# Performance work log

Measured on AMD Instinct MI355X. Metric: run time of the kernel, lower is better.

Reference implementation:

```python
import jax, jax.numpy as jnp
import numpy as np

K, T, CIN = 30000, 35, 7
EPS = 1e-5  # torch BatchNorm default


def _bn(x, gamma, beta):
    # x: [1, K, T, C]; per-channel batch-stat normalization over (0,1,2)
    mean = jnp.mean(x, axis=(0, 1, 2))
    var = jnp.var(x, axis=(0, 1, 2))
    return (x - mean) * jax.lax.rsqrt(var + EPS) * gamma + beta


def _vfe(x, mask, W, b, gamma, beta):
    # x: [1, K, T, Cin] -> [1, K, T, 2*units]
    pw = jnp.einsum('bkti,iu->bktu', x, W) + b
    pw = jax.nn.relu(_bn(pw, gamma, beta))
    agg = jnp.max(pw, axis=2, keepdims=True)            # [1, K, 1, units]
    out = jnp.concatenate([pw, jnp.broadcast_to(agg, pw.shape)], axis=-1)
    return out * mask


def setup_inputs() -> dict:
    key = jax.random.key(0)
    ks = jax.random.split(key, 8)
    inp = {}
    inp['x'] = jax.random.normal(ks[0], (K, T, CIN), jnp.float32)
    inp['coordinate'] = jax.random.randint(ks[1], (K, 4), 0, 1, dtype=jnp.int32)
    inp['batch_size'] = 1
    inp['W1'] = jax.random.normal(ks[2], (7, 16), jnp.float32) * 0.3
    inp['b1'] = jnp.zeros((16,), jnp.float32)
    inp['g1'] = jnp.ones((16,), jnp.float32)
    inp['be1'] = jnp.zeros((16,), jnp.float32)
    inp['W2'] = jax.random.normal(ks[3], (32, 64), jnp.float32) * 0.15
    inp['b2'] = jnp.zeros((64,), jnp.float32)
    inp['g2'] = jnp.ones((64,), jnp.float32)
    inp['be2'] = jnp.zeros((64,), jnp.float32)
    inp['Wd'] = jax.random.normal(ks[4], (128, 128), jnp.float32) * 0.1
    inp['bd'] = jnp.zeros((128,), jnp.float32)
    inp['gd'] = jnp.ones((128,), jnp.float32)
    inp['bed'] = jnp.zeros((128,), jnp.float32)
    return inp


def reference(x, coordinate, batch_size, W1, b1, g1, be1, W2, b2, g2, be2, Wd, bd, gd, bed):
    xb = x[None]                                   # [1, K, T, 7]
    # mask: 1 where the point's feature sum is nonzero
    mask = (jnp.sum(xb, axis=-1) != 0.0).astype(jnp.float32)[..., None]  # [1,K,T,1]
    h = _vfe(xb, mask, W1, b1, g1, be1)            # [1, K, T, 32]
    h = _vfe(h, mask, W2, b2, g2, be2)             # [1, K, T, 128]
    h = jnp.einsum('bktc,cd->bktd', h, Wd) + bd    # [1, K, T, 128]
    h = _bn(h, gd, bed)                            # BatchNorm2d after permute(0,3,1,2)
    h = jnp.where(h >= 0, h, 0.1 * h)              # leaky_relu(0.1)
    h = jnp.max(h, axis=2)                         # max over points -> [1, K, 128]
    out = jnp.transpose(h, (0, 2, 1))              # [1, 128, K] to match NCHW layout
    return (out, coordinate)
```

## Files before the change

kernel.cpp:

```cpp
#include <hip/hip_runtime.h>

#define KVOX 30000
#define TP 35
#define NPTS (KVOX * TP)
#define EPS_BN 1e-5f

typedef __attribute__((ext_vector_type(8))) short short8_t;
typedef __attribute__((ext_vector_type(4))) float f32x4;

#define MFMA_BF16 __builtin_amdgcn_mfma_f32_16x16x32_bf16

#define SLOTG_OFF 0
#define SLOT2_OFF 2560
#define SLOT3_OFF 10752
#define PAR_A1 27136
#define PAR_C1 27152
#define PAR_A2 27168
#define PAR_C2 27232
#define PAR_A3 27296
#define PAR_C3 27424
#define STATS_FLOATS 27136
#define W2T_OFF 27552
#define WDT_OFF 28576
#define M3_OFF 36768
#define SMALL_FLOATS (36768 + KVOX * 64)
#define H1G_OFF SMALL_FLOATS
#define REC_DW 1224
#define FULL_FLOATS (H1G_OFF + (KVOX / 4) * REC_DW)

__device__ __forceinline__ ushort f2bf(float f) {
    uint r;
    asm("v_cvt_pk_bf16_f32 %0, %1, %2" : "=v"(r) : "v"(f), "v"(f));
    return (ushort)r;
}
__device__ __forceinline__ uint f2bf2(float lo, float hi) {
    uint r;
    asm("v_cvt_pk_bf16_f32 %0, %1, %2" : "=v"(r) : "v"(lo), "v"(hi));
    return r;
}
__device__ __forceinline__ float bf2f(ushort h) {
    union { uint u; float f; } v; v.u = ((uint)h) << 16; return v.f;
}

__global__ __launch_bounds__(256) void k_prep_stats1(
    const float* __restrict__ x,
    const float* __restrict__ W2, const float* __restrict__ Wd,
    const float* __restrict__ gd,
    ushort* __restrict__ w2t, ushort* __restrict__ wdt,
    float* __restrict__ slotG) {
    if (blockIdx.x < 64) {
        int t = blockIdx.x * 256 + threadIdx.x;
        if (t < 2048) {
            int u = t >> 5, k = t & 31;
            w2t[t] = f2bf(W2[k * 64 + u]);
        }
        int u = t >> 7, k = t & 127;
        float sg = (gd[u] < 0.f) ? -1.f : 1.f;
        wdt[t] = f2bf(Wd[k * 128 + u] * sg);
        return;
    }
    int bid = blockIdx.x - 64;
    int tid = threadIdx.x;
    int gid = bid * 256 + tid;
    float sx[7], G[28];
#pragma unroll
    for (int c = 0; c < 7; ++c) sx[c] = 0.f;
#pragma unroll
    for (int i = 0; i < 28; ++i) G[i] = 0.f;
    for (size_t p4 = (size_t)gid * 4; p4 < NPTS; p4 += (size_t)65536 * 4) {
        const f32x4* xp = (const f32x4*)(x + p4 * 7);
        f32x4 q[7];
#pragma unroll
        for (int c = 0; c < 7; ++c) q[c] = xp[c];
#pragma unroll
        for (int j = 0; j < 4; ++j) {
            float xv[7];
#pragma unroll
            for (int c = 0; c < 7; ++c) {
                int idx = j * 7 + c;
                xv[c] = q[idx >> 2][idx & 3];
                sx[c] += xv[c];
            }
            int idx = 0;
#pragma unroll
            for (int i = 0; i < 7; ++i)
#pragma unroll
                for (int jj = i; jj < 7; ++jj) { G[idx] = fmaf(xv[i], xv[jj], G[idx]); ++idx; }
        }
    }
    int lane = tid & 63;
    int wv = tid >> 6;
    int slot = (bid * 4 + wv) & 63;
#pragma unroll
    for (int k = 0; k < 35; ++k) {
        float v = (k < 28) ? G[k] : sx[k - 28];
#pragma unroll
        for (int m = 32; m > 0; m >>= 1) v += __shfl_xor(v, m, 64);
        if (lane == 0) atomicAdd(&slotG[slot * 40 + k], v);
    }
}

__global__ void k_affine1g(const float* __restrict__ slotG,
                           const float* __restrict__ W1, const float* __restrict__ b1,
                           const float* __restrict__ g1, const float* __restrict__ be1,
                           float* __restrict__ pa, float* __restrict__ pc, float invN) {
    __shared__ float red[35];
    int t = threadIdx.x;
    if (t < 35) {
        float s = 0.f;
#pragma unroll
        for (int sl = 0; sl < 64; ++sl) s += slotG[sl * 40 + t];
        red[t] = s;
    }
    __syncthreads();
    if (t < 16) {
        float wv[7];
#pragma unroll
        for (int c = 0; c < 7; ++c) wv[c] = W1[c * 16 + t];
        float b = b1[t];
        float sw = 0.f;
#pragma unroll
        for (int c = 0; c < 7; ++c) sw = fmaf(red[28 + c], wv[c], sw);
        float gq = 0.f;
        int idx = 0;
#pragma unroll
        for (int i = 0; i < 7; ++i)
#pragma unroll
            for (int j = i; j < 7; ++j) {
                float coef = wv[i] * wv[j];
                if (i != j) coef *= 2.f;
                gq = fmaf(coef, red[idx], gq);
                ++idx;
            }
        float mr = sw * invN;
        float mean = mr + b;
        float ex2 = gq * invN + 2.f * b * mr + b * b;
        float var = ex2 - mean * mean;
        float av = g1[t] * rsqrtf(var + EPS_BN);
        pa[t] = av;
        pc[t] = be1[t] - mean * av;
    }
}

__global__ void k_affine_b(const float* __restrict__ slots,
                           const float* __restrict__ g,
                           const float* __restrict__ be,
                           const float* __restrict__ bias,
                           float* __restrict__ pa, float* __restrict__ pc,
                           int C, float invN) {
    int u = threadIdx.x;
    if (u >= C) return;
    float s = 0.f, q = 0.f;
    for (int sl = 0; sl < 64; ++sl) {
        s += slots[sl * 2 * C + u];
        q += slots[sl * 2 * C + C + u];
    }
    float b = bias[u];
    float mr = s * invN;
    float mean = mr + b;
    float ex2 = q * invN + 2.f * b * mr + b * b;
    float var = ex2 - mean * mean;
    float av = g[u] * rsqrtf(var + EPS_BN);
    pa[u] = av;
    pc[u] = be[u] - mean * av;
}

__global__ void k_affine_b3(const float* __restrict__ slots,
                            const float* __restrict__ g,
                            const float* __restrict__ be,
                            const float* __restrict__ bias,
                            float* __restrict__ pa, float* __restrict__ pc,
                            int C, float invN) {
    int u = threadIdx.x;
    if (u >= C) return;
    float s = 0.f, q = 0.f;
    for (int sl = 0; sl < 64; ++sl) {
        s += slots[sl * 2 * C + u];
        q += slots[sl * 2 * C + C + u];
    }
    float sg = (g[u] < 0.f) ? -1.f : 1.f;
    s *= sg;
    float b = bias[u];
    float mr = s * invN;
    float mean = mr + b;
    float ex2 = q * invN + 2.f * b * mr + b * b;
    float var = ex2 - mean * mean;
    float av = g[u] * rsqrtf(var + EPS_BN);
    pa[u] = av;
    pc[u] = be[u] - mean * av;
}

__device__ __forceinline__ void phaseA4(
    int k0, int tid,
    const float* __restrict__ x,
    const float* __restrict__ W1, const float* __restrict__ b1,
    const float* __restrict__ a1, const float* __restrict__ c1,
    ushort* __restrict__ h1, float* __restrict__ lmask,
    float* __restrict__ aggp , ushort* __restrict__ agg1bf ) {
    int u = tid & 15;
    int g = tid >> 4;
    int v = g & 3;
    int th = g >> 2;
    float pmax = 0.f;
    if (th < 7) {
        float b1u = b1[u];
        float a1u = a1[u], c1u = c1[u];
        float w1c[7];
#pragma unroll
        for (int c = 0; c < 7; ++c) w1c[c] = W1[c * 16 + u];
#pragma unroll
        for (int i = 0; i < 5; ++i) {
            int t = th * 5 + i;
            const float* xp = x + ((size_t)(k0 + v) * TP + t) * 7;
            float xv[7];
            float sum7 = 0.f;
#pragma unroll
            for (int c = 0; c < 7; ++c) { xv[c] = xp[c]; sum7 += xv[c]; }
            float mkv = (sum7 != 0.f) ? 1.f : 0.f;
            int row = 4 * t + v;
            if (u == 0) lmask[row] = mkv;
            float val = b1u;
#pragma unroll
            for (int c = 0; c < 7; ++c) val = fmaf(xv[c], w1c[c], val);
            val = fmaxf(fmaf(a1u, val, c1u), 0.f);
            pmax = fmaxf(pmax, val);
            h1[row * 24 + u] = f2bf(val * mkv);
        }
    } else {
        int row = 140 + v;
        h1[row * 24 + u] = 0;
        if (u == 0) lmask[row] = 0.f;
    }
    int w = tid >> 6;
    int lane = tid & 63;
    if (w < 7) aggp[w * 64 + lane] = pmax;
    __syncthreads();
    if (tid < 64) {
        float m = aggp[tid];
#pragma unroll
        for (int ww = 1; ww < 7; ++ww) m = fmaxf(m, aggp[ww * 64 + tid]);
        agg1bf[tid] = f2bf(m);
    }
    __syncthreads();
}

template <bool DUMP>
__global__ __launch_bounds__(512, 8) void k_stats2(
    const float* __restrict__ x,
    const float* __restrict__ W1, const float* __restrict__ b1,
    const ushort* __restrict__ w2t,
    const float* __restrict__ ws,
    float* __restrict__ slot2, uint* __restrict__ recs) {
    __shared__ __align__(16) ushort h1[144 * 24];
    __shared__ float lmask[144];
    __shared__ float aggp[7 * 64];
    __shared__ __align__(16) ushort agg1bf[64];
    __shared__ __align__(16) uint zeros16[4];
    int tid = threadIdx.x;
    int k0 = blockIdx.x * 4;
    if (tid < 4) zeros16[tid] = 0;
    phaseA4(k0, tid, x, W1, b1, ws + PAR_A1, ws + PAR_C1, h1, lmask, aggp, agg1bf);
    if (DUMP) {
        uint* rec = recs + (size_t)blockIdx.x * REC_DW;
        const uint* h1dw = (const uint*)h1;
        for (int i = tid; i < 1120; i += 512) rec[i] = h1dw[(i >> 3) * 12 + (i & 7)];
        if (tid < 32) rec[1120 + tid] = ((const uint*)agg1bf)[tid];
        if (tid < 70) rec[1152 + tid] = f2bf2(lmask[2 * tid], lmask[2 * tid + 1]);
    }
    int w = tid >> 6, lane = tid & 63, lq = lane >> 4, lr = lane & 15;
    int mh = w >> 2, uq = w & 3;
    int u = uq * 16 + lr;
    short8_t bB = *(const short8_t*)(w2t + u * 32 + (lq & 1) * 8);
    short8_t bP = *(const short8_t*)(w2t + u * 32 + 16 + (lq & 1) * 8);
    const ushort* pap = (lq < 2) ? (agg1bf + (lr & 3) * 16 + (lq & 1) * 8) : (const ushort*)zeros16;
    short8_t pAf = *(const short8_t*)pap;
    f32x4 aP = {0.f, 0.f, 0.f, 0.f};
    aP = MFMA_BF16(pAf, bP, aP, 0, 0, 0);
    f32x4 p1;
    p1[0] = __shfl(aP[0], lr, 64); p1[1] = __shfl(aP[1], lr, 64);
    p1[2] = __shfl(aP[2], lr, 64); p1[3] = __shfl(aP[3], lr, 64);
    f32x4 s1p = {0.f, 0.f, 0.f, 0.f}, s2p = {0.f, 0.f, 0.f, 0.f};
    int mt0 = mh ? 5 : 0, mt1 = mh ? 9 : 5;
    for (int mt = mt0; mt < mt1; ++mt) {
        const ushort* ha = (lq < 2) ? (h1 + (mt * 16 + lr) * 24 + (lq & 1) * 8) : (const ushort*)zeros16;
        short8_t af = *(const short8_t*)ha;
        f32x4 acc = {0.f, 0.f, 0.f, 0.f};
        acc = MFMA_BF16(af, bB, acc, 0, 0, 0);
        f32x4 mk = *(const f32x4*)(lmask + mt * 16 + lq * 4);
        f32x4 am = (acc + p1) * mk;
        s1p += am;
        s2p += am * am;
    }
    float s1 = s1p[0] + s1p[1] + s1p[2] + s1p[3];
    float s2 = s2p[0] + s2p[1] + s2p[2] + s2p[3];
    s1 += __shfl_xor(s1, 16, 64); s1 += __shfl_xor(s1, 32, 64);
    s2 += __shfl_xor(s2, 16, 64); s2 += __shfl_xor(s2, 32, 64);
    if (lq == 0) {
        int slot = blockIdx.x & 63;
        atomicAdd(&slot2[slot * 128 + u], s1);
        atomicAdd(&slot2[slot * 128 + 64 + u], s2);
    }
}

__global__ __launch_bounds__(512, 8) void k_stage3_reuse(
    const uint* __restrict__ recs,
    const float* __restrict__ b2,
    const ushort* __restrict__ w2t, const ushort* __restrict__ wdt,
    const float* __restrict__ bd, const float* __restrict__ gd,
    const float* __restrict__ ws,
    float* __restrict__ slot3, ushort* __restrict__ m3) {
    __shared__ __align__(16) ushort h1[144 * 24];
    __shared__ __align__(16) ushort h2[144 * 72];
    __shared__ float lmask[144];
    __shared__ __align__(16) uint aggfU[4 * 68];
    __shared__ __align__(16) ushort agg1bf[64];
    __shared__ __align__(16) uint zeros16[4];
    int tid = threadIdx.x;
    int k0 = blockIdx.x * 4;
    int w = tid >> 6, lane = tid & 63, lq = lane >> 4, lr = lane & 15;

    {
        const uint* rec = recs + (size_t)blockIdx.x * REC_DW;
        uint* h1dw = (uint*)h1;
        {
            int i = tid;              h1dw[(i >> 3) * 12 + (i & 7)] = rec[i];
            i = tid + 512;            h1dw[(i >> 3) * 12 + (i & 7)] = rec[i];
            i = tid + 1024; if (i < 1120) h1dw[(i >> 3) * 12 + (i & 7)] = rec[i];
        }
        if (tid < 48) h1dw[140 * 12 + tid] = 0u;
        if (tid < 32) ((uint*)agg1bf)[tid] = rec[1120 + tid];
        if (tid < 72) {
            if (tid < 70) {
                uint mw = rec[1152 + tid];
                lmask[2 * tid] = bf2f((ushort)(mw & 0xffffu));
                lmask[2 * tid + 1] = bf2f((ushort)(mw >> 16));
            } else {
                int j = 140 + (tid - 70) * 2;
                lmask[j] = 0.f; lmask[j + 1] = 0.f;
            }
        }
        if (tid < 272) aggfU[tid] = 0u;
        if (tid < 4) zeros16[tid] = 0u;
    }
    __syncthreads();

    {
        int mh = w >> 2, uq = w & 3;
        int u = uq * 16 + lr;
        short8_t bB = *(const short8_t*)(w2t + u * 32 + (lq & 1) * 8);
        short8_t bP = *(const short8_t*)(w2t + u * 32 + 16 + (lq & 1) * 8);
        const ushort* pap = (lq < 2) ? (agg1bf + (lr & 3) * 16 + (lq & 1) * 8) : (const ushort*)zeros16;
        short8_t pAf = *(const short8_t*)pap;
        f32x4 aP = {0.f, 0.f, 0.f, 0.f};
        aP = MFMA_BF16(pAf, bP, aP, 0, 0, 0);
        f32x4 p1;
        p1[0] = __shfl(aP[0], lr, 64); p1[1] = __shfl(aP[1], lr, 64);
        p1[2] = __shfl(aP[2], lr, 64); p1[3] = __shfl(aP[3], lr, 64);
        float a2u = ws[PAR_A2 + u];
        float c2u = fmaf(a2u, b2[u], ws[PAR_C2 + u]);
        f32x4 av = {0.f, 0.f, 0.f, 0.f};
        int mt0 = mh ? 5 : 0, mt1 = mh ? 9 : 5;
        for (int mt = mt0; mt < mt1; ++mt) {
            const ushort* ha = (lq < 2) ? (h1 + (mt * 16 + lr) * 24 + (lq & 1) * 8) : (const ushort*)zeros16;
            short8_t af = *(const short8_t*)ha;
            f32x4 acc = {0.f, 0.f, 0.f, 0.f};
            acc = MFMA_BF16(af, bB, acc, 0, 0, 0);
            f32x4 mk = *(const f32x4*)(lmask + mt * 16 + lq * 4);
            int m0 = mt * 16 + lq * 4;
            f32x4 vals;
#pragma unroll
            for (int r = 0; r < 4; ++r) {
                float am = (acc[r] + p1[r]) * mk[r];
                float val = fmaxf(fmaf(a2u, am, c2u), 0.f);
                h2[(m0 + r) * 72 + u] = f2bf(val);
                vals[r] = val;
            }
            if (!(mt == 8 && lq == 3)) {
#pragma unroll
                for (int r = 0; r < 4; ++r) av[r] = fmaxf(av[r], vals[r]);
            }
        }
#pragma unroll
        for (int r = 0; r < 4; ++r) {
            av[r] = fmaxf(av[r], __shfl_xor(av[r], 16, 64));
            av[r] = fmaxf(av[r], __shfl_xor(av[r], 32, 64));
        }
        if (lq == 0) {
#pragma unroll
            for (int r = 0; r < 4; ++r)
                atomicMax(&aggfU[r * 68 + u], __float_as_uint(av[r]));
        }
    }
    __syncthreads();

    {
        int u = w * 16 + lr;
        short8_t bM0 = *(const short8_t*)(wdt + u * 128 + lq * 8);
        short8_t bM1 = *(const short8_t*)(wdt + u * 128 + 32 + lq * 8);
        short8_t bP0 = *(const short8_t*)(wdt + u * 128 + 64 + lq * 8);
        short8_t bP1 = *(const short8_t*)(wdt + u * 128 + 96 + lq * 8);
        const float* aggf = (const float*)aggfU;
        f32x4 q0 = *(const f32x4*)(aggf + (lr & 3) * 68 + lq * 8);
        f32x4 q1 = *(const f32x4*)(aggf + (lr & 3) * 68 + lq * 8 + 4);
        f32x4 q2 = *(const f32x4*)(aggf + (lr & 3) * 68 + 32 + lq * 8);
        f32x4 q3 = *(const f32x4*)(aggf + (lr & 3) * 68 + 32 + lq * 8 + 4);
        union { uint uu[4]; short8_t s8; } pc0, pc1;
        pc0.uu[0] = f2bf2(q0[0], q0[1]); pc0.uu[1] = f2bf2(q0[2], q0[3]);
        pc0.uu[2] = f2bf2(q1[0], q1[1]); pc0.uu[3] = f2bf2(q1[2], q1[3]);
        pc1.uu[0] = f2bf2(q2[0], q2[1]); pc1.uu[1] = f2bf2(q2[2], q2[3]);
        pc1.uu[2] = f2bf2(q3[0], q3[1]); pc1.uu[3] = f2bf2(q3[2], q3[3]);
        f32x4 aP = {0.f, 0.f, 0.f, 0.f};
        aP = MFMA_BF16(pc0.s8, bP0, aP, 0, 0, 0);
        aP = MFMA_BF16(pc1.s8, bP1, aP, 0, 0, 0);
        f32x4 p2;
        p2[0] = __shfl(aP[0], lr, 64); p2[1] = __shfl(aP[1], lr, 64);
        p2[2] = __shfl(aP[2], lr, 64); p2[3] = __shfl(aP[3], lr, 64);
        f32x4 s1p = {0.f, 0.f, 0.f, 0.f}, s2p = {0.f, 0.f, 0.f, 0.f};
        f32x4 mx = {-1e30f, -1e30f, -1e30f, -1e30f};
#pragma unroll
        for (int mt = 0; mt < 9; ++mt) {
            const ushort* hrow = h2 + (mt * 16 + lr) * 72;
            short8_t a0 = *(const short8_t*)(hrow + lq * 8);
            short8_t a1 = *(const short8_t*)(hrow + 32 + lq * 8);
            f32x4 acc = {0.f, 0.f, 0.f, 0.f};
            acc = MFMA_BF16(a0, bM0, acc, 0, 0, 0);
            acc = MFMA_BF16(a1, bM1, acc, 0, 0, 0);
            f32x4 mk = *(const f32x4*)(lmask + mt * 16 + lq * 4);
            f32x4 am = (acc + p2) * mk;
            s1p += am;
            s2p += am * am;
            if (mt < 8) {
#pragma unroll
                for (int r = 0; r < 4; ++r) mx[r] = fmaxf(mx[r], am[r]);
            } else if (lq < 3) {
#pragma unroll
                for (int r = 0; r < 4; ++r) mx[r] = fmaxf(mx[r], am[r]);
            }
        }
#pragma unroll
        for (int r = 0; r < 4; ++r) {
            mx[r] = fmaxf(mx[r], __shfl_xor(mx[r], 16, 64));
            mx[r] = fmaxf(mx[r], __shfl_xor(mx[r], 32, 64));
        }
        float s1 = s1p[0] + s1p[1] + s1p[2] + s1p[3];
        float s2 = s2p[0] + s2p[1] + s2p[2] + s2p[3];
        s1 += __shfl_xor(s1, 16, 64); s1 += __shfl_xor(s1, 32, 64);
        s2 += __shfl_xor(s2, 16, 64); s2 += __shfl_xor(s2, 32, 64);
        if (lq == 0) {
            float sg = (gd[u] < 0.f) ? -1.f : 1.f;
            float bdu = bd[u];
#pragma unroll
            for (int r = 0; r < 4; ++r)
                m3[(size_t)(k0 + r) * 128 + u] = f2bf(fmaf(sg, mx[r], bdu));
            int slot = blockIdx.x & 63;
            atomicAdd(&slot3[slot * 256 + u], s1);
            atomicAdd(&slot3[slot * 256 + 128 + u], s2);
        }
    }
}

__device__ __forceinline__ void phaseA_leg(
    int k0, int tid,
    const float* __restrict__ x,
    const float* __restrict__ W1, const float* __restrict__ b1,
    const float* __restrict__ a1, const float* __restrict__ c1,
    ushort* __restrict__ h1, float* __restrict__ lmask, float* __restrict__ aggp) {
    int u = tid & 15;
    int g = tid >> 4;
    int v = g & 1;
    int th = g >> 1;
    float pmax = 0.f;
    if (th < 7) {
        float b1u = b1[u];
        float a1u = a1[u], c1u = c1[u];
        float w1c[7];
#pragma unroll
        for (int c = 0; c < 7; ++c) w1c[c] = W1[c * 16 + u];
#pragma unroll
        for (int i = 0; i < 5; ++i) {
            int t = th * 5 + i;
            const float* xp = x + ((size_t)(k0 + v) * TP + t) * 7;
            float xv[7];
            float sum7 = 0.f;
#pragma unroll
            for (int c = 0; c < 7; ++c) { xv[c] = xp[c]; sum7 += xv[c]; }
            float mkv = (sum7 != 0.f) ? 1.f : 0.f;
            if (u == 0) lmask[v * TP + t] = mkv;
            float val = b1u;
#pragma unroll
            for (int c = 0; c < 7; ++c) val = fmaf(xv[c], w1c[c], val);
            val = fmaxf(fmaf(a1u, val, c1u), 0.f);
            pmax = fmaxf(pmax, val);
            h1[(v * TP + t) * 40 + u] = f2bf(val * mkv);
        }
    } else {
#pragma unroll
        for (int i = 0; i < 5; ++i) {
            int row = 70 + (g & 1) * 5 + i;
            h1[row * 40 + u] = 0;
            if (u == 0) lmask[row] = 0.f;
        }
    }
    pmax = fmaxf(pmax, __shfl_xor(pmax, 32, 64));
    int w = tid >> 6;
    int lane = tid & 63;
    if (lane < 32) aggp[w * 32 + lane] = pmax;
    __syncthreads();
    {
        int uu = tid & 15;
        int r0 = tid >> 4;
        float g0 = fmaxf(fmaxf(aggp[uu], aggp[32 + uu]),
                         fmaxf(aggp[64 + uu], aggp[96 + uu]));
        float g1 = fmaxf(fmaxf(aggp[16 + uu], aggp[48 + uu]),
                         fmaxf(aggp[80 + uu], aggp[112 + uu]));
        ushort a0 = f2bf(g0), a1b = f2bf(g1);
#pragma unroll
        for (int j = 0; j < 5; ++j) {
            int row = r0 + j * 16;
            float mkv = lmask[row];
            h1[row * 40 + 16 + uu] = (mkv != 0.f) ? ((row < TP) ? a0 : a1b) : (ushort)0;
        }
    }
    __syncthreads();
}

template <bool WSPATH>
__global__ __launch_bounds__(256) void k_stage3_full(
    const float* __restrict__ x,
    const float* __restrict__ W1, const float* __restrict__ b1,
    const float* __restrict__ b2,
    const ushort* __restrict__ w2t, const ushort* __restrict__ wdt,
    const float* __restrict__ bd, const float* __restrict__ gd,
    const float* __restrict__ ws,
    float* __restrict__ slot3,
    ushort* __restrict__ m3, float* __restrict__ outbuf) {
    __shared__ __align__(16) ushort h1[80 * 40];
    __shared__ __align__(16) ushort h2[80 * 136];
    __shared__ float lmask[80];
    __shared__ float aggp[128];
    __shared__ ushort agg2bf[128];
    int tid = threadIdx.x;
    int k0 = blockIdx.x * 2;
    int w = tid >> 6, lane = tid & 63, lq = lane >> 4, lr = lane & 15;
    phaseA_leg(k0, tid, x, W1, b1, ws + PAR_A1, ws + PAR_C1, h1, lmask, aggp);

    int u0 = w * 32;
    short8_t bfr[2][4];
#pragma unroll
    for (int s = 0; s < 2; ++s)
#pragma unroll
        for (int kk = 0; kk < 4; ++kk)
            bfr[s][kk] = *(const short8_t*)(wdt + ((u0 + s * 16 + lr) * 128 + kk * 32 + lq * 8));

    {
        int u = w * 16 + lr;
        short8_t bfrag = *(const short8_t*)(w2t + u * 32 + lq * 8);
        float a2u = ws[PAR_A2 + u];
        float c2p = fmaf(a2u, b2[u], ws[PAR_C2 + u]);
        float aggv0 = 0.f, aggv1 = 0.f;
#pragma unroll
        for (int mt = 0; mt < 5; ++mt) {
            short8_t afrag = *(const short8_t*)(h1 + (mt * 16 + lr) * 40 + lq * 8);
            f32x4 acc = {0.f, 0.f, 0.f, 0.f};
            acc = MFMA_BF16(afrag, bfrag, acc, 0, 0, 0);
#pragma unroll
            for (int r = 0; r < 4; ++r) {
                int m = mt * 16 + lq * 4 + r;
                float val = fmaxf(fmaf(a2u, acc[r], c2p), 0.f);
                float vm = (m < 70) ? val : 0.f;
                if (m < TP) aggv0 = fmaxf(aggv0, vm); else aggv1 = fmaxf(aggv1, vm);
                h2[m * 136 + u] = f2bf(val * lmask[m]);
            }
        }
        aggv0 = fmaxf(aggv0, __shfl_xor(aggv0, 16, 64));
        aggv0 = fmaxf(aggv0, __shfl_xor(aggv0, 32, 64));
        aggv1 = fmaxf(aggv1, __shfl_xor(aggv1, 16, 64));
        aggv1 = fmaxf(aggv1, __shfl_xor(aggv1, 32, 64));
        if (lq == 0) {
            agg2bf[u] = f2bf(aggv0);
            agg2bf[64 + u] = f2bf(aggv1);
        }
    }
    __syncthreads();
    {
        int c = tid & 63;
        int r0 = tid >> 6;
        ushort a0 = agg2bf[c], a1v = agg2bf[64 + c];
#pragma unroll
        for (int j = 0; j < 20; ++j) {
            int row = r0 + j * 4;
            float mkv = lmask[row];
            h2[row * 136 + 64 + c] = (mkv != 0.f) ? ((row < TP) ? a0 : a1v) : (ushort)0;
        }
    }
    __syncthreads();
    {
        float mxa[2][2], s1a[2], s2a[2];
#pragma unroll
        for (int s = 0; s < 2; ++s) {
            s1a[s] = 0.f; s2a[s] = 0.f;
            mxa[s][0] = -1e30f; mxa[s][1] = -1e30f;
        }
#pragma unroll
        for (int mt = 0; mt < 5; ++mt) {
            short8_t af[4];
#pragma unroll
            for (int kk = 0; kk < 4; ++kk)
                af[kk] = *(const short8_t*)(h2 + (mt * 16 + lr) * 136 + kk * 32 + lq * 8);
#pragma unroll
            for (int s = 0; s < 2; ++s) {
                f32x4 acc = {0.f, 0.f, 0.f, 0.f};
#pragma unroll
                for (int kk = 0; kk < 4; ++kk)
                    acc = MFMA_BF16(af[kk], bfr[s][kk], acc, 0, 0, 0);
#pragma unroll
                for (int r = 0; r < 4; ++r) {
                    float a = acc[r];
                    s1a[s] += a;
                    s2a[s] = fmaf(a, a, s2a[s]);
                    int m = mt * 16 + lq * 4 + r;
                    if (mt <= 1) mxa[s][0] = fmaxf(mxa[s][0], a);
                    else if (mt == 3) mxa[s][1] = fmaxf(mxa[s][1], a);
                    else if (mt == 2) { if (m < TP) mxa[s][0] = fmaxf(mxa[s][0], a); else mxa[s][1] = fmaxf(mxa[s][1], a); }
                    else { if (m < 70) mxa[s][1] = fmaxf(mxa[s][1], a); }
                }
            }
        }
#pragma unroll
        for (int s = 0; s < 2; ++s) {
#pragma unroll
            for (int v = 0; v < 2; ++v) {
                mxa[s][v] = fmaxf(mxa[s][v], __shfl_xor(mxa[s][v], 16, 64));
                mxa[s][v] = fmaxf(mxa[s][v], __shfl_xor(mxa[s][v], 32, 64));
            }
            s1a[s] += __shfl_xor(s1a[s], 16, 64); s1a[s] += __shfl_xor(s1a[s], 32, 64);
            s2a[s] += __shfl_xor(s2a[s], 16, 64); s2a[s] += __shfl_xor(s2a[s], 32, 64);
        }
        if (lq == 0) {
            int slot = blockIdx.x & 63;
#pragma unroll
            for (int s = 0; s < 2; ++s) {
                int u = u0 + s * 16 + lr;
                float bdu = bd[u];
                float sg = (gd[u] < 0.f) ? -1.f : 1.f;
#pragma unroll
                for (int v = 0; v < 2; ++v) {
                    float res = fmaf(sg, mxa[s][v], bdu);
                    if (WSPATH) m3[(size_t)(k0 + v) * 128 + u] = f2bf(res);
                    else        outbuf[(size_t)u * KVOX + (k0 + v)] = res;
                }
                atomicAdd(&slot3[slot * 256 + u], s1a[s]);
                atomicAdd(&slot3[slot * 256 + 128 + u], s2a[s]);
            }
        }
    }
}

__global__ __launch_bounds__(256) void k_final_ws(const ushort* __restrict__ m3,
                                                  const float* __restrict__ ws,
                                                  float* __restrict__ out) {
    __shared__ float tile[32][33];
    int tx = threadIdx.x & 31;
    int ty = threadIdx.x >> 5;
    int v0 = blockIdx.x * 32;
    int u0 = blockIdx.y * 32;
    const float* a3 = ws + PAR_A3;
    const float* c3 = ws + PAR_C3;
#pragma unroll
    for (int r = ty; r < 32; r += 8) {
        int v = v0 + r, u = u0 + tx;
        float y = 0.f;
        if (v < KVOX) {
            float a = a3[u], c = c3[u];
            float val = bf2f(m3[(size_t)v * 128 + u]);
            y = a * val + c;
            y = (y >= 0.f) ? y : 0.1f * y;
        }
        tile[r][tx] = y;
    }
    __syncthreads();
#pragma unroll
    for (int r = ty; r < 32; r += 8) {
        int u = u0 + r, v = v0 + tx;
        if (v < KVOX) out[(size_t)u * KVOX + v] = tile[tx][r];
    }
}

__global__ __launch_bounds__(256) void k_final_inplace(const float* __restrict__ ws,
                                                       float* __restrict__ out) {
    int v = blockIdx.x * 256 + threadIdx.x;
    int u = blockIdx.y;
    if (v >= KVOX) return;
    float a = ws[PAR_A3 + u], c = ws[PAR_C3 + u];
    size_t idx = (size_t)u * KVOX + v;
    float y = a * out[idx] + c;
    out[idx] = (y >= 0.f) ? y : 0.1f * y;
}

extern "C" void kernel_launch(void* const* d_in, const int* in_sizes, int n_in,
                              void* d_out, int out_size, void* d_ws, size_t ws_size,
                              hipStream_t stream) {
    const float* x   = (const float*)d_in[0];
    const void*  coord = d_in[1];
    const float* W1  = (const float*)d_in[3];
    const float* b1  = (const float*)d_in[4];
    const float* g1  = (const float*)d_in[5];
    const float* be1 = (const float*)d_in[6];
    const float* W2  = (const float*)d_in[7];
    const float* b2  = (const float*)d_in[8];
    const float* g2  = (const float*)d_in[9];
    const float* be2 = (const float*)d_in[10];
    const float* Wd  = (const float*)d_in[11];
    const float* bd  = (const float*)d_in[12];
    const float* gd  = (const float*)d_in[13];
    const float* bed = (const float*)d_in[14];
    float* ws = (float*)d_ws;
    float* out = (float*)d_out;
    ushort* w2t = (ushort*)(ws + W2T_OFF);
    ushort* wdt = (ushort*)(ws + WDT_OFF);
    ushort* m3  = (ushort*)(ws + M3_OFF);
    uint* recs  = (uint*)(ws + H1G_OFF);

    size_t wsf = ws_size / 4;
    bool full = wsf >= (size_t)FULL_FLOATS;
    bool small = wsf >= (size_t)SMALL_FLOATS;
    const float invN = 1.f / (float)NPTS;

    hipMemsetAsync(d_ws, 0, (size_t)STATS_FLOATS * 4, stream);

    k_prep_stats1<<<64 + 256, 256, 0, stream>>>(x, W2, Wd, gd, w2t, wdt, ws + SLOTG_OFF);
    k_affine1g<<<1, 64, 0, stream>>>(ws + SLOTG_OFF, W1, b1, g1, be1, ws + PAR_A1, ws + PAR_C1, invN);
    if (full)
        k_stats2<true><<<KVOX / 4, 512, 0, stream>>>(x, W1, b1, w2t, ws, ws + SLOT2_OFF, recs);
    else
        k_stats2<false><<<KVOX / 4, 512, 0, stream>>>(x, W1, b1, w2t, ws, ws + SLOT2_OFF, recs);
    k_affine_b<<<1, 64, 0, stream>>>(ws + SLOT2_OFF, g2, be2, b2, ws + PAR_A2, ws + PAR_C2, 64, invN);

    if (full) {
        k_stage3_reuse<<<KVOX / 4, 512, 0, stream>>>(recs, b2, w2t, wdt, bd, gd, ws,
                                                     ws + SLOT3_OFF, m3);
        k_affine_b3<<<1, 128, 0, stream>>>(ws + SLOT3_OFF, gd, bed, bd, ws + PAR_A3, ws + PAR_C3, 128, invN);
        k_final_ws<<<dim3((KVOX + 31) / 32, 4), 256, 0, stream>>>(m3, ws, out);
    } else if (small) {
        k_stage3_full<true><<<KVOX / 2, 256, 0, stream>>>(x, W1, b1, b2, w2t, wdt, bd, gd, ws,
                                                          ws + SLOT3_OFF, m3, out);
        k_affine_b3<<<1, 128, 0, stream>>>(ws + SLOT3_OFF, gd, bed, bd, ws + PAR_A3, ws + PAR_C3, 128, invN);
        k_final_ws<<<dim3((KVOX + 31) / 32, 4), 256, 0, stream>>>(m3, ws, out);
    } else {
        k_stage3_full<false><<<KVOX / 2, 256, 0, stream>>>(x, W1, b1, b2, w2t, wdt, bd, gd, ws,
                                                           ws + SLOT3_OFF, m3, out);
        k_affine_b3<<<1, 128, 0, stream>>>(ws + SLOT3_OFF, gd, bed, bd, ws + PAR_A3, ws + PAR_C3, 128, invN);
        k_final_inplace<<<dim3((KVOX + 255) / 256, 128), 256, 0, stream>>>(ws, out);
    }
    hipMemcpyAsync((char*)d_out + (size_t)128 * KVOX * 4, coord,
                   (size_t)KVOX * 4 * sizeof(int), hipMemcpyDeviceToDevice, stream);
}
```

Before: 154.0 us.

## Fuse stats and stage kernels into one persistent kernel with grid barriers

```diff
diff --git a/kernel.cpp b/kernel.cpp
--- a/kernel.cpp
+++ b/kernel.cpp
@@ -4,6 +4,9 @@
 #define TP 35
 #define NPTS (KVOX * TP)
 #define EPS_BN 1e-5f
+#define NBLK 768
+#define GRP 10
+#define TOTG 7500
 
 typedef __attribute__((ext_vector_type(8))) short short8_t;
 typedef __attribute__((ext_vector_type(4))) float f32x4;
@@ -13,20 +16,20 @@
 #define SLOTG_OFF 0
 #define SLOT2_OFF 2560
 #define SLOT3_OFF 10752
-#define PAR_A1 27136
-#define PAR_C1 27152
-#define PAR_A2 27168
-#define PAR_C2 27232
-#define PAR_A3 27296
-#define PAR_C3 27424
-#define STATS_FLOATS 27136
-#define W2T_OFF 27552
-#define WDT_OFF 28576
-#define M3_OFF 36768
-#define SMALL_FLOATS (36768 + KVOX * 64)
-#define H1G_OFF SMALL_FLOATS
-#define REC_DW 1224
-#define FULL_FLOATS (H1G_OFF + (KVOX / 4) * REC_DW)
+#define BAR_OFF   27136
+#define PAR_A1 27152
+#define PAR_C1 27168
+#define PAR_A2 27184
+#define PAR_C2 27248
+#define PAR_A3 27312
+#define PAR_C3 27440
+#define STATS_FLOATS 27568
+#define W2T_OFF 27568
+#define WDT_OFF 28592
+#define M3_OFF 36784
+#define SMALL_FLOATS (36784 + KVOX * 64)
+#define RECS_OFF SMALL_FLOATS
+#define FULL_FLOATS (RECS_OFF + TOTG * 1120)
 
 __device__ __forceinline__ ushort f2bf(float f) {
     uint r;
@@ -41,25 +44,434 @@
 __device__ __forceinline__ float bf2f(ushort h) {
     union { uint u; float f; } v; v.u = ((uint)h) << 16; return v.f;
 }
-
-__global__ __launch_bounds__(256) void k_prep_stats1(
+__device__ __forceinline__ float aload(const float* p) {
+    return __hip_atomic_load(p, __ATOMIC_RELAXED, __HIP_MEMORY_SCOPE_AGENT);
+}
+__device__ __forceinline__ void gbar(uint* c, uint nblk) {
+    __syncthreads();
+    if (threadIdx.x == 0) {
+        __threadfence();
+        __hip_atomic_fetch_add(c, 1u, __ATOMIC_RELEASE, __HIP_MEMORY_SCOPE_AGENT);
+        while (__hip_atomic_load(c, __ATOMIC_ACQUIRE, __HIP_MEMORY_SCOPE_AGENT) < nblk)
+            __builtin_amdgcn_s_sleep(1);
+        __threadfence();
+    }
+    __syncthreads();
+}
+
+__global__ __launch_bounds__(256) void k_prep(const float* __restrict__ W2,
+                                              const float* __restrict__ Wd,
+                                              const float* __restrict__ gd,
+                                              ushort* __restrict__ w2t,
+                                              ushort* __restrict__ wdt) {
+    int t = blockIdx.x * 256 + threadIdx.x;
+    if (t < 2048) {
+        int u = t >> 5, k = t & 31;
+        w2t[t] = f2bf(W2[k * 64 + u]);
+    }
+    int u = t >> 7, k = t & 127;
+    float sg = (gd[u] < 0.f) ? -1.f : 1.f;
+    wdt[t] = f2bf(Wd[k * 128 + u] * sg);
+}
+
+__global__ __launch_bounds__(512, 8) void k_fused(
     const float* __restrict__ x,
-    const float* __restrict__ W2, const float* __restrict__ Wd,
-    const float* __restrict__ gd,
-    ushort* __restrict__ w2t, ushort* __restrict__ wdt,
-    float* __restrict__ slotG) {
-    if (blockIdx.x < 64) {
-        int t = blockIdx.x * 256 + threadIdx.x;
-        if (t < 2048) {
-            int u = t >> 5, k = t & 31;
-            w2t[t] = f2bf(W2[k * 64 + u]);
-        }
-        int u = t >> 7, k = t & 127;
-        float sg = (gd[u] < 0.f) ? -1.f : 1.f;
-        wdt[t] = f2bf(Wd[k * 128 + u] * sg);
-        return;
-    }
-    int bid = blockIdx.x - 64;
+    const float* __restrict__ W1, const float* __restrict__ b1,
+    const float* __restrict__ g1, const float* __restrict__ be1,
+    const float* __restrict__ b2, const float* __restrict__ g2,
+    const float* __restrict__ be2,
+    const ushort* __restrict__ w2t, const ushort* __restrict__ wdt,
+    const float* __restrict__ bd, const float* __restrict__ gd,
+    float* __restrict__ slotG, float* __restrict__ slot2,
+    float* __restrict__ slot3,
+    uint* __restrict__ bar, uint* __restrict__ recs,
+    ushort* __restrict__ m3) {
+    __shared__ __align__(16) ushort h1[144 * 24];
+    __shared__ __align__(16) ushort h2[144 * 72];
+    __shared__ __align__(16) float lmask[GRP][144];
+    __shared__ __align__(16) ushort agg1[GRP][64];
+    __shared__ __align__(16) uint aggfU[2][272];
+    __shared__ float parA1[16], parC1[16], parA2[64], parC2[64];
+    __shared__ __align__(16) uint zeros16[4];
+    float* aggp = (float*)h2;
+
+    const float invN = 1.f / (float)NPTS;
+    int tid = threadIdx.x;
+    int b = blockIdx.x;
+    int w = tid >> 6, lane = tid & 63, lq = lane >> 4, lr = lane & 15;
+
+    if (tid < 4) zeros16[tid] = 0u;
+    for (int j = tid; j < GRP * 144; j += 512) ((float*)lmask)[j] = 0.f;
+    if (tid < 64) h1[(140 + (tid >> 4)) * 24 + (tid & 15)] = 0;
+
+    {
+        float sx[7], G[28];
+#pragma unroll
+        for (int c = 0; c < 7; ++c) sx[c] = 0.f;
+#pragma unroll
+        for (int i = 0; i < 28; ++i) G[i] = 0.f;
+        int gid = b * 512 + tid;
+        if (gid < NPTS / 4) {
+            const float* xp = x + (size_t)gid * 28;
+#pragma unroll
+            for (int j = 0; j < 4; ++j) {
+                float xv[7];
+#pragma unroll
+                for (int c = 0; c < 7; ++c) { xv[c] = xp[j * 7 + c]; sx[c] += xv[c]; }
+                int idx = 0;
+#pragma unroll
+                for (int ii = 0; ii < 7; ++ii)
+#pragma unroll
+                    for (int jj = ii; jj < 7; ++jj) {
+                        G[idx] = fmaf(xv[ii], xv[jj], G[idx]); ++idx;
+                    }
+            }
+        }
+        int slot = (b * 8 + w) & 63;
+#pragma unroll
+        for (int k = 0; k < 35; ++k) {
+            float v = (k < 28) ? G[k] : sx[k - 28];
+#pragma unroll
+            for (int m = 32; m > 0; m >>= 1) v += __shfl_xor(v, m, 64);
+            if (lane == 0) atomicAdd(&slotG[slot * 40 + k], v);
+        }
+    }
+    gbar(&bar[0], NBLK);
+
+    if (tid < 35) {
+        float s = 0.f;
+#pragma unroll
+        for (int sl = 0; sl < 64; ++sl) s += aload(&slotG[sl * 40 + tid]);
+        aggp[tid] = s;
+    }
+    __syncthreads();
+    if (tid < 16) {
+        float wv[7];
+#pragma unroll
+        for (int c = 0; c < 7; ++c) wv[c] = W1[c * 16 + tid];
+        float bq = b1[tid];
+        float sw = 0.f;
+#pragma unroll
+        for (int c = 0; c < 7; ++c) sw = fmaf(aggp[28 + c], wv[c], sw);
+        float gq = 0.f;
+        int idx = 0;
+#pragma unroll
+        for (int ii = 0; ii < 7; ++ii)
+#pragma unroll
+            for (int jj = ii; jj < 7; ++jj) {
+                float coef = wv[ii] * wv[jj];
+                if (ii != jj) coef *= 2.f;
+                gq = fmaf(coef, aggp[idx], gq);
+                ++idx;
+            }
+        float mr = sw * invN;
+        float mean = mr + bq;
+        float ex2 = gq * invN + 2.f * bq * mr + bq * bq;
+        float var = ex2 - mean * mean;
+        float av = g1[tid] * rsqrtf(var + EPS_BN);
+        parA1[tid] = av;
+        parC1[tid] = be1[tid] - mean * av;
+    }
+    __syncthreads();
+
+    for (int i = 0; i < GRP; ++i) {
+        int g = b * GRP + i;
+        bool act = g < TOTG;
+        int k0 = g * 4;
+        if (act) {
+            int u = tid & 15, gg = tid >> 4, v = gg & 3, th = gg >> 2;
+            float pmax = 0.f;
+            if (th < 7) {
+                float b1u = b1[u];
+                float a1u = parA1[u], c1u = parC1[u];
+                float w1c[7];
+#pragma unroll
+                for (int c = 0; c < 7; ++c) w1c[c] = W1[c * 16 + u];
+#pragma unroll
+                for (int ii = 0; ii < 5; ++ii) {
+                    int t = th * 5 + ii;
+                    const float* xp = x + ((size_t)(k0 + v) * TP + t) * 7;
+                    float xv[7];
+                    float sum7 = 0.f;
+#pragma unroll
+                    for (int c = 0; c < 7; ++c) { xv[c] = xp[c]; sum7 += xv[c]; }
+                    float mkv = (sum7 != 0.f) ? 1.f : 0.f;
+                    int row = 4 * t + v;
+                    if (u == 0) lmask[i][row] = mkv;
+                    float val = b1u;
+#pragma unroll
+                    for (int c = 0; c < 7; ++c) val = fmaf(xv[c], w1c[c], val);
+                    val = fmaxf(fmaf(a1u, val, c1u), 0.f);
+                    pmax = fmaxf(pmax, val);
+                    h1[row * 24 + u] = f2bf(val * mkv);
+                }
+            }
+            if (w < 7) aggp[w * 64 + lane] = pmax;
+        }
+        __syncthreads();
+        if (act && tid < 64) {
+            float m = aggp[tid];
+#pragma unroll
+            for (int ww = 1; ww < 7; ++ww) m = fmaxf(m, aggp[ww * 64 + tid]);
+            agg1[i][tid] = f2bf(m);
+        }
+        __syncthreads();
+        if (act) {
+            const uint* h1dw = (const uint*)h1;
+            uint* rec = recs + (size_t)g * 1120;
+            {
+                int j = tid;            rec[j] = h1dw[(j >> 3) * 12 + (j & 7)];
+                j = tid + 512;          rec[j] = h1dw[(j >> 3) * 12 + (j & 7)];
+                j = tid + 1024; if (j < 1120) rec[j] = h1dw[(j >> 3) * 12 + (j & 7)];
+            }
+            int mh = w >> 2, uq = w & 3;
+            int u = uq * 16 + lr;
+            short8_t bB = *(const short8_t*)(w2t + u * 32 + (lq & 1) * 8);
+            short8_t bP = *(const short8_t*)(w2t + u * 32 + 16 + (lq & 1) * 8);
+            const ushort* pap = (lq < 2) ? (&agg1[i][0] + (lr & 3) * 16 + (lq & 1) * 8)
+                                         : (const ushort*)zeros16;
+            short8_t pAf = *(const short8_t*)pap;
+            f32x4 aP = {0.f, 0.f, 0.f, 0.f};
+            aP = MFMA_BF16(pAf, bP, aP, 0, 0, 0);
+            f32x4 p1;
+            p1[0] = __shfl(aP[0], lr, 64); p1[1] = __shfl(aP[1], lr, 64);
+            p1[2] = __shfl(aP[2], lr, 64); p1[3] = __shfl(aP[3], lr, 64);
+            f32x4 s1p = {0.f, 0.f, 0.f, 0.f}, s2p = {0.f, 0.f, 0.f, 0.f};
+            int mt0 = mh ? 5 : 0, mt1 = mh ? 9 : 5;
+            for (int mt = mt0; mt < mt1; ++mt) {
+                const ushort* ha = (lq < 2) ? (h1 + (mt * 16 + lr) * 24 + (lq & 1) * 8)
+                                            : (const ushort*)zeros16;
+                short8_t af = *(const short8_t*)ha;
+                f32x4 acc = {0.f, 0.f, 0.f, 0.f};
+                acc = MFMA_BF16(af, bB, acc, 0, 0, 0);
+                f32x4 mk = *(const f32x4*)(&lmask[i][mt * 16 + lq * 4]);
+                f32x4 am = (acc + p1) * mk;
+                s1p += am;
+                s2p += am * am;
+            }
+            float s1 = s1p[0] + s1p[1] + s1p[2] + s1p[3];
+            float s2 = s2p[0] + s2p[1] + s2p[2] + s2p[3];
+            s1 += __shfl_xor(s1, 16, 64); s1 += __shfl_xor(s1, 32, 64);
+            s2 += __shfl_xor(s2, 16, 64); s2 += __shfl_xor(s2, 32, 64);
+            if (lq == 0) {
+                int slot = g & 63;
+                atomicAdd(&slot2[slot * 128 + u], s1);
+                atomicAdd(&slot2[slot * 128 + 64 + u], s2);
+            }
+        }
+        __syncthreads();
+    }
+    gbar(&bar[1], NBLK);
+
+    if (tid < 64) {
+        float s = 0.f, q = 0.f;
+#pragma unroll
+        for (int sl = 0; sl < 64; ++sl) {
+            s += aload(&slot2[sl * 128 + tid]);
+            q += aload(&slot2[sl * 128 + 64 + tid]);
+        }
+        float bq = b2[tid];
+        float mr = s * invN;
+        float mean = mr + bq;
+        float ex2 = q * invN + 2.f * bq * mr + bq * bq;
+        float var = ex2 - mean * mean;
+        float av = g2[tid] * rsqrtf(var + EPS_BN);
+        parA2[tid] = av;
+        parC2[tid] = fmaf(av, bq, be2[tid] - mean * av);
+    }
+    __syncthreads();
+
+    for (int i = 0; i < GRP; ++i) {
+        int g = b * GRP + i;
+        bool act = g < TOTG;
+        int k0 = g * 4;
+        uint* afU = aggfU[i & 1];
+        if (act) {
+            uint* h1dw = (uint*)h1;
+            const uint* rec = recs + (size_t)g * 1120;
+            {
+                int j = tid;            h1dw[(j >> 3) * 12 + (j & 7)] = rec[j];
+                j = tid + 512;          h1dw[(j >> 3) * 12 + (j & 7)] = rec[j];
+                j = tid + 1024; if (j < 1120) h1dw[(j >> 3) * 12 + (j & 7)] = rec[j];
+            }
+            if (tid < 272) afU[tid] = 0u;
+        }
+        __syncthreads();
+        if (act) {
+            int mh = w >> 2, uq = w & 3;
+            int u = uq * 16 + lr;
+            short8_t bB = *(const short8_t*)(w2t + u * 32 + (lq & 1) * 8);
+            short8_t bP = *(const short8_t*)(w2t + u * 32 + 16 + (lq & 1) * 8);
+            const ushort* pap = (lq < 2) ? (&agg1[i][0] + (lr & 3) * 16 + (lq & 1) * 8)
+                                         : (const ushort*)zeros16;
+            short8_t pAf = *(const short8_t*)pap;
+            f32x4 aP = {0.f, 0.f, 0.f, 0.f};
+            aP = MFMA_BF16(pAf, bP, aP, 0, 0, 0);
+            f32x4 p1;
+            p1[0] = __shfl(aP[0], lr, 64); p1[1] = __shfl(aP[1], lr, 64);
+            p1[2] = __shfl(aP[2], lr, 64); p1[3] = __shfl(aP[3], lr, 64);
+            float a2u = parA2[u];
+            float c2u = parC2[u];
+            f32x4 av = {0.f, 0.f, 0.f, 0.f};
+            int mt0 = mh ? 5 : 0, mt1 = mh ? 9 : 5;
+            for (int mt = mt0; mt < mt1; ++mt) {
+                const ushort* ha = (lq < 2) ? (h1 + (mt * 16 + lr) * 24 + (lq & 1) * 8)
+                                            : (const ushort*)zeros16;
+                short8_t af = *(const short8_t*)ha;
+                f32x4 acc = {0.f, 0.f, 0.f, 0.f};
+                acc = MFMA_BF16(af, bB, acc, 0, 0, 0);
+                f32x4 mk = *(const f32x4*)(&lmask[i][mt * 16 + lq * 4]);
+                int m0 = mt * 16 + lq * 4;
+                f32x4 vals;
+#pragma unroll
+                for (int r = 0; r < 4; ++r) {
+                    float am = (acc[r] + p1[r]) * mk[r];
+                    float val = fmaxf(fmaf(a2u, am, c2u), 0.f);
+                    h2[(m0 + r) * 72 + u] = f2bf(val);
+                    vals[r] = val;
+                }
+                if (!(mt == 8 && lq == 3)) {
+#pragma unroll
+                    for (int r = 0; r < 4; ++r) av[r] = fmaxf(av[r], vals[r]);
+                }
+            }
+#pragma unroll
+            for (int r = 0; r < 4; ++r) {
+                av[r] = fmaxf(av[r], __shfl_xor(av[r], 16, 64));
+                av[r] = fmaxf(av[r], __shfl_xor(av[r], 32, 64));
+            }
+            if (lq == 0) {
+#pragma unroll
+                for (int r = 0; r < 4; ++r)
+                    atomicMax(&afU[r * 68 + u], __float_as_uint(av[r]));
+            }
+        }
+        __syncthreads();
+        if (act) {
+            int u = w * 16 + lr;
+            short8_t bM0 = *(const short8_t*)(wdt + u * 128 + lq * 8);
+            short8_t bM1 = *(const short8_t*)(wdt + u * 128 + 32 + lq * 8);
+            short8_t bP0 = *(const short8_t*)(wdt + u * 128 + 64 + lq * 8);
+            short8_t bP1 = *(const short8_t*)(wdt + u * 128 + 96 + lq * 8);
+            const float* aggf = (const float*)afU;
+            f32x4 q0 = *(const f32x4*)(aggf + (lr & 3) * 68 + lq * 8);
+            f32x4 q1 = *(const f32x4*)(aggf + (lr & 3) * 68 + lq * 8 + 4);
+            f32x4 q2 = *(const f32x4*)(aggf + (lr & 3) * 68 + 32 + lq * 8);
+            f32x4 q3 = *(const f32x4*)(aggf + (lr & 3) * 68 + 32 + lq * 8 + 4);
+            union { uint uu[4]; short8_t s8; } pc0, pc1;
+            pc0.uu[0] = f2bf2(q0[0], q0[1]); pc0.uu[1] = f2bf2(q0[2], q0[3]);
+            pc0.uu[2] = f2bf2(q1[0], q1[1]); pc0.uu[3] = f2bf2(q1[2], q1[3]);
+            pc1.uu[0] = f2bf2(q2[0], q2[1]); pc1.uu[1] = f2bf2(q2[2], q2[3]);
+            pc1.uu[2] = f2bf2(q3[0], q3[1]); pc1.uu[3] = f2bf2(q3[2], q3[3]);
+            f32x4 aP = {0.f, 0.f, 0.f, 0.f};
+            aP = MFMA_BF16(pc0.s8, bP0, aP, 0, 0, 0);
+            aP = MFMA_BF16(pc1.s8, bP1, aP, 0, 0, 0);
+            f32x4 p2;
+            p2[0] = __shfl(aP[0], lr, 64); p2[1] = __shfl(aP[1], lr, 64);
+            p2[2] = __shfl(aP[2], lr, 64); p2[3] = __shfl(aP[3], lr, 64);
+            f32x4 s1p = {0.f, 0.f, 0.f, 0.f}, s2p = {0.f, 0.f, 0.f, 0.f};
+            f32x4 mx = {-1e30f, -1e30f, -1e30f, -1e30f};
+#pragma unroll
+            for (int mt = 0; mt < 9; ++mt) {
+                const ushort* hrow = h2 + (mt * 16 + lr) * 72;
+                short8_t a0 = *(const short8_t*)(hrow + lq * 8);
+                short8_t a1 = *(const short8_t*)(hrow + 32 + lq * 8);
+                f32x4 acc = {0.f, 0.f, 0.f, 0.f};
+                acc = MFMA_BF16(a0, bM0, acc, 0, 0, 0);
+                acc = MFMA_BF16(a1, bM1, acc, 0, 0, 0);
+                f32x4 mk = *(const f32x4*)(&lmask[i][mt * 16 + lq * 4]);
+                f32x4 am = (acc + p2) * mk;
+                s1p += am;
+                s2p += am * am;
+                if (mt < 8) {
+#pragma unroll
+                    for (int r = 0; r < 4; ++r) mx[r] = fmaxf(mx[r], am[r]);
+                } else if (lq < 3) {
+#pragma unroll
+                    for (int r = 0; r < 4; ++r) mx[r] = fmaxf(mx[r], am[r]);
+                }
+            }
+#pragma unroll
+            for (int r = 0; r < 4; ++r) {
+                mx[r] = fmaxf(mx[r], __shfl_xor(mx[r], 16, 64));
+                mx[r] = fmaxf(mx[r], __shfl_xor(mx[r], 32, 64));
+            }
+            float s1 = s1p[0] + s1p[1] + s1p[2] + s1p[3];
+            float s2 = s2p[0] + s2p[1] + s2p[2] + s2p[3];
+            s1 += __shfl_xor(s1, 16, 64); s1 += __shfl_xor(s1, 32, 64);
+            s2 += __shfl_xor(s2, 16, 64); s2 += __shfl_xor(s2, 32, 64);
+            if (lq == 0) {
+                float sg = (gd[u] < 0.f) ? -1.f : 1.f;
+                float bdu = bd[u];
+#pragma unroll
+                for (int r = 0; r < 4; ++r)
+                    m3[(size_t)(k0 + r) * 128 + u] = f2bf(fmaf(sg, mx[r], bdu));
+                int slot = g & 63;
+                atomicAdd(&slot3[slot * 256 + u], s1);
+                atomicAdd(&slot3[slot * 256 + 128 + u], s2);
+            }
+        }
+    }
+}
+
+__global__ void k_affine_b3(const float* __restrict__ slots,
+                            const float* __restrict__ g,
+                            const float* __restrict__ be,
+                            const float* __restrict__ bias,
+                            float* __restrict__ pa, float* __restrict__ pc,
+                            int C, float invN) {
+    int u = threadIdx.x;
+    if (u >= C) return;
+    float s = 0.f, q = 0.f;
+    for (int sl = 0; sl < 64; ++sl) {
+        s += slots[sl * 2 * C + u];
+        q += slots[sl * 2 * C + C + u];
+    }
+    float sg = (g[u] < 0.f) ? -1.f : 1.f;
+    s *= sg;
+    float b = bias[u];
+    float mr = s * invN;
+    float mean = mr + b;
+    float ex2 = q * invN + 2.f * b * mr + b * b;
+    float var = ex2 - mean * mean;
+    float av = g[u] * rsqrtf(var + EPS_BN);
+    pa[u] = av;
+    pc[u] = be[u] - mean * av;
+}
+
+__global__ __launch_bounds__(256) void k_final_ws(const ushort* __restrict__ m3,
+                                                  const float* __restrict__ ws,
+                                                  float* __restrict__ out) {
+    __shared__ float tile[32][33];
+    int tx = threadIdx.x & 31;
+    int ty = threadIdx.x >> 5;
+    int v0 = blockIdx.x * 32;
+    int u0 = blockIdx.y * 32;
+    const float* a3 = ws + PAR_A3;
+    const float* c3 = ws + PAR_C3;
+#pragma unroll
+    for (int r = ty; r < 32; r += 8) {
+        int v = v0 + r, u = u0 + tx;
+        float y = 0.f;
+        if (v < KVOX) {
+            float a = a3[u], c = c3[u];
+            float val = bf2f(m3[(size_t)v * 128 + u]);
+            y = a * val + c;
+            y = (y >= 0.f) ? y : 0.1f * y;
+        }
+        tile[r][tx] = y;
+    }
+    __syncthreads();
+#pragma unroll
+    for (int r = ty; r < 32; r += 8) {
+        int u = u0 + r, v = v0 + tx;
+        if (v < KVOX) out[(size_t)u * KVOX + v] = tile[tx][r];
+    }
+}
+
+__global__ __launch_bounds__(256) void k_gram(const float* __restrict__ x,
+                                              float* __restrict__ slotG) {
+    int bid = blockIdx.x;
     int tid = threadIdx.x;
     int gid = bid * 256 + tid;
     float sx[7], G[28];
@@ -68,24 +480,17 @@
 #pragma unroll
     for (int i = 0; i < 28; ++i) G[i] = 0.f;
     for (size_t p4 = (size_t)gid * 4; p4 < NPTS; p4 += (size_t)65536 * 4) {
-        const f32x4* xp = (const f32x4*)(x + p4 * 7);
-        f32x4 q[7];
-#pragma unroll
-        for (int c = 0; c < 7; ++c) q[c] = xp[c];
+        const float* xp = x + p4 * 7;
 #pragma unroll
         for (int j = 0; j < 4; ++j) {
             float xv[7];
 #pragma unroll
-            for (int c = 0; c < 7; ++c) {
-                int idx = j * 7 + c;
-                xv[c] = q[idx >> 2][idx & 3];
-                sx[c] += xv[c];
-            }
+            for (int c = 0; c < 7; ++c) { xv[c] = xp[j * 7 + c]; sx[c] += xv[c]; }
             int idx = 0;
 #pragma unroll
-            for (int i = 0; i < 7; ++i)
-#pragma unroll
-                for (int jj = i; jj < 7; ++jj) { G[idx] = fmaf(xv[i], xv[jj], G[idx]); ++idx; }
+            for (int ii = 0; ii < 7; ++ii)
+#pragma unroll
+                for (int jj = ii; jj < 7; ++jj) { G[idx] = fmaf(xv[ii], xv[jj], G[idx]); ++idx; }
         }
     }
     int lane = tid & 63;
@@ -163,300 +568,6 @@
     float av = g[u] * rsqrtf(var + EPS_BN);
     pa[u] = av;
     pc[u] = be[u] - mean * av;
-}
-
-__global__ void k_affine_b3(const float* __restrict__ slots,
-                            const float* __restrict__ g,
-                            const float* __restrict__ be,
-                            const float* __restrict__ bias,
-                            float* __restrict__ pa, float* __restrict__ pc,
-                            int C, float invN) {
-    int u = threadIdx.x;
-    if (u >= C) return;
-    float s = 0.f, q = 0.f;
-    for (int sl = 0; sl < 64; ++sl) {
-        s += slots[sl * 2 * C + u];
-        q += slots[sl * 2 * C + C + u];
-    }
-    float sg = (g[u] < 0.f) ? -1.f : 1.f;
-    s *= sg;
-    float b = bias[u];
-    float mr = s * invN;
-    float mean = mr + b;
-    float ex2 = q * invN + 2.f * b * mr + b * b;
-    float var = ex2 - mean * mean;
-    float av = g[u] * rsqrtf(var + EPS_BN);
-    pa[u] = av;
-    pc[u] = be[u] - mean * av;
-}
-
-__device__ __forceinline__ void phaseA4(
-    int k0, int tid,
-    const float* __restrict__ x,
-    const float* __restrict__ W1, const float* __restrict__ b1,
-    const float* __restrict__ a1, const float* __restrict__ c1,
-    ushort* __restrict__ h1, float* __restrict__ lmask,
-    float* __restrict__ aggp , ushort* __restrict__ agg1bf ) {
-    int u = tid & 15;
-    int g = tid >> 4;
-    int v = g & 3;
-    int th = g >> 2;
-    float pmax = 0.f;
-    if (th < 7) {
-        float b1u = b1[u];
-        float a1u = a1[u], c1u = c1[u];
-        float w1c[7];
-#pragma unroll
-        for (int c = 0; c < 7; ++c) w1c[c] = W1[c * 16 + u];
-#pragma unroll
-        for (int i = 0; i < 5; ++i) {
-            int t = th * 5 + i;
-            const float* xp = x + ((size_t)(k0 + v) * TP + t) * 7;
-            float xv[7];
-            float sum7 = 0.f;
-#pragma unroll
-            for (int c = 0; c < 7; ++c) { xv[c] = xp[c]; sum7 += xv[c]; }
-            float mkv = (sum7 != 0.f) ? 1.f : 0.f;
-            int row = 4 * t + v;
-            if (u == 0) lmask[row] = mkv;
-            float val = b1u;
-#pragma unroll
-            for (int c = 0; c < 7; ++c) val = fmaf(xv[c], w1c[c], val);
-            val = fmaxf(fmaf(a1u, val, c1u), 0.f);
-            pmax = fmaxf(pmax, val);
-            h1[row * 24 + u] = f2bf(val * mkv);
-        }
-    } else {
-        int row = 140 + v;
-        h1[row * 24 + u] = 0;
-        if (u == 0) lmask[row] = 0.f;
-    }
-    int w = tid >> 6;
-    int lane = tid & 63;
-    if (w < 7) aggp[w * 64 + lane] = pmax;
-    __syncthreads();
-    if (tid < 64) {
-        float m = aggp[tid];
-#pragma unroll
-        for (int ww = 1; ww < 7; ++ww) m = fmaxf(m, aggp[ww * 64 + tid]);
-        agg1bf[tid] = f2bf(m);
-    }
-    __syncthreads();
-}
-
-template <bool DUMP>
-__global__ __launch_bounds__(512, 8) void k_stats2(
-    const float* __restrict__ x,
-    const float* __restrict__ W1, const float* __restrict__ b1,
-    const ushort* __restrict__ w2t,
-    const float* __restrict__ ws,
-    float* __restrict__ slot2, uint* __restrict__ recs) {
-    __shared__ __align__(16) ushort h1[144 * 24];
-    __shared__ float lmask[144];
-    __shared__ float aggp[7 * 64];
-    __shared__ __align__(16) ushort agg1bf[64];
-    __shared__ __align__(16) uint zeros16[4];
-    int tid = threadIdx.x;
-    int k0 = blockIdx.x * 4;
-    if (tid < 4) zeros16[tid] = 0;
-    phaseA4(k0, tid, x, W1, b1, ws + PAR_A1, ws + PAR_C1, h1, lmask, aggp, agg1bf);
-    if (DUMP) {
-        uint* rec = recs + (size_t)blockIdx.x * REC_DW;
-        const uint* h1dw = (const uint*)h1;
-        for (int i = tid; i < 1120; i += 512) rec[i] = h1dw[(i >> 3) * 12 + (i & 7)];
-        if (tid < 32) rec[1120 + tid] = ((const uint*)agg1bf)[tid];
-        if (tid < 70) rec[1152 + tid] = f2bf2(lmask[2 * tid], lmask[2 * tid + 1]);
-    }
-    int w = tid >> 6, lane = tid & 63, lq = lane >> 4, lr = lane & 15;
-    int mh = w >> 2, uq = w & 3;
-    int u = uq * 16 + lr;
-    short8_t bB = *(const short8_t*)(w2t + u * 32 + (lq & 1) * 8);
-    short8_t bP = *(const short8_t*)(w2t + u * 32 + 16 + (lq & 1) * 8);
-    const ushort* pap = (lq < 2) ? (agg1bf + (lr & 3) * 16 + (lq & 1) * 8) : (const ushort*)zeros16;
-    short8_t pAf = *(const short8_t*)pap;
-    f32x4 aP = {0.f, 0.f, 0.f, 0.f};
-    aP = MFMA_BF16(pAf, bP, aP, 0, 0, 0);
-    f32x4 p1;
-    p1[0] = __shfl(aP[0], lr, 64); p1[1] = __shfl(aP[1], lr, 64);
-    p1[2] = __shfl(aP[2], lr, 64); p1[3] = __shfl(aP[3], lr, 64);
-    f32x4 s1p = {0.f, 0.f, 0.f, 0.f}, s2p = {0.f, 0.f, 0.f, 0.f};
-    int mt0 = mh ? 5 : 0, mt1 = mh ? 9 : 5;
-    for (int mt = mt0; mt < mt1; ++mt) {
-        const ushort* ha = (lq < 2) ? (h1 + (mt * 16 + lr) * 24 + (lq & 1) * 8) : (const ushort*)zeros16;
-        short8_t af = *(const short8_t*)ha;
-        f32x4 acc = {0.f, 0.f, 0.f, 0.f};
-        acc = MFMA_BF16(af, bB, acc, 0, 0, 0);
-        f32x4 mk = *(const f32x4*)(lmask + mt * 16 + lq * 4);
-        f32x4 am = (acc + p1) * mk;
-        s1p += am;
-        s2p += am * am;
-    }
-    float s1 = s1p[0] + s1p[1] + s1p[2] + s1p[3];
-    float s2 = s2p[0] + s2p[1] + s2p[2] + s2p[3];
-    s1 += __shfl_xor(s1, 16, 64); s1 += __shfl_xor(s1, 32, 64);
-    s2 += __shfl_xor(s2, 16, 64); s2 += __shfl_xor(s2, 32, 64);
-    if (lq == 0) {
-        int slot = blockIdx.x & 63;
-        atomicAdd(&slot2[slot * 128 + u], s1);
-        atomicAdd(&slot2[slot * 128 + 64 + u], s2);
-    }
-}
-
-__global__ __launch_bounds__(512, 8) void k_stage3_reuse(
-    const uint* __restrict__ recs,
-    const float* __restrict__ b2,
-    const ushort* __restrict__ w2t, const ushort* __restrict__ wdt,
-    const float* __restrict__ bd, const float* __restrict__ gd,
-    const float* __restrict__ ws,
-    float* __restrict__ slot3, ushort* __restrict__ m3) {
-    __shared__ __align__(16) ushort h1[144 * 24];
-    __shared__ __align__(16) ushort h2[144 * 72];
-    __shared__ float lmask[144];
-    __shared__ __align__(16) uint aggfU[4 * 68];
-    __shared__ __align__(16) ushort agg1bf[64];
-    __shared__ __align__(16) uint zeros16[4];
-    int tid = threadIdx.x;
-    int k0 = blockIdx.x * 4;
-    int w = tid >> 6, lane = tid & 63, lq = lane >> 4, lr = lane & 15;
-
-    {
-        const uint* rec = recs + (size_t)blockIdx.x * REC_DW;
-        uint* h1dw = (uint*)h1;
-        {
-            int i = tid;              h1dw[(i >> 3) * 12 + (i & 7)] = rec[i];
-            i = tid + 512;            h1dw[(i >> 3) * 12 + (i & 7)] = rec[i];
-            i = tid + 1024; if (i < 1120) h1dw[(i >> 3) * 12 + (i & 7)] = rec[i];
-        }
-        if (tid < 48) h1dw[140 * 12 + tid] = 0u;
-        if (tid < 32) ((uint*)agg1bf)[tid] = rec[1120 + tid];
-        if (tid < 72) {
-            if (tid < 70) {
-                uint mw = rec[1152 + tid];
-                lmask[2 * tid] = bf2f((ushort)(mw & 0xffffu));
-                lmask[2 * tid + 1] = bf2f((ushort)(mw >> 16));
-            } else {
-                int j = 140 + (tid - 70) * 2;
-                lmask[j] = 0.f; lmask[j + 1] = 0.f;
-            }
-        }
-        if (tid < 272) aggfU[tid] = 0u;
-        if (tid < 4) zeros16[tid] = 0u;
-    }
-    __syncthreads();
-
-    {
-        int mh = w >> 2, uq = w & 3;
-        int u = uq * 16 + lr;
-        short8_t bB = *(const short8_t*)(w2t + u * 32 + (lq & 1) * 8);
-        short8_t bP = *(const short8_t*)(w2t + u * 32 + 16 + (lq & 1) * 8);
-        const ushort* pap = (lq < 2) ? (agg1bf + (lr & 3) * 16 + (lq & 1) * 8) : (const ushort*)zeros16;
-        short8_t pAf = *(const short8_t*)pap;
-        f32x4 aP = {0.f, 0.f, 0.f, 0.f};
-        aP = MFMA_BF16(pAf, bP, aP, 0, 0, 0);
-        f32x4 p1;
-        p1[0] = __shfl(aP[0], lr, 64); p1[1] = __shfl(aP[1], lr, 64);
-        p1[2] = __shfl(aP[2], lr, 64); p1[3] = __shfl(aP[3], lr, 64);
-        float a2u = ws[PAR_A2 + u];
-        float c2u = fmaf(a2u, b2[u], ws[PAR_C2 + u]);
-        f32x4 av = {0.f, 0.f, 0.f, 0.f};
-        int mt0 = mh ? 5 : 0, mt1 = mh ? 9 : 5;
-        for (int mt = mt0; mt < mt1; ++mt) {
-            const ushort* ha = (lq < 2) ? (h1 + (mt * 16 + lr) * 24 + (lq & 1) * 8) : (const ushort*)zeros16;
-            short8_t af = *(const short8_t*)ha;
-            f32x4 acc = {0.f, 0.f, 0.f, 0.f};
-            acc = MFMA_BF16(af, bB, acc, 0, 0, 0);
-            f32x4 mk = *(const f32x4*)(lmask + mt * 16 + lq * 4);
-            int m0 = mt * 16 + lq * 4;
-            f32x4 vals;
-#pragma unroll
-            for (int r = 0; r < 4; ++r) {
-                float am = (acc[r] + p1[r]) * mk[r];
-                float val = fmaxf(fmaf(a2u, am, c2u), 0.f);
-                h2[(m0 + r) * 72 + u] = f2bf(val);
-                vals[r] = val;
-            }
-            if (!(mt == 8 && lq == 3)) {
-#pragma unroll
-                for (int r = 0; r < 4; ++r) av[r] = fmaxf(av[r], vals[r]);
-            }
-        }
-#pragma unroll
-        for (int r = 0; r < 4; ++r) {
-            av[r] = fmaxf(av[r], __shfl_xor(av[r], 16, 64));
-            av[r] = fmaxf(av[r], __shfl_xor(av[r], 32, 64));
-        }
-        if (lq == 0) {
-#pragma unroll
-            for (int r = 0; r < 4; ++r)
-                atomicMax(&aggfU[r * 68 + u], __float_as_uint(av[r]));
-        }
-    }
-    __syncthreads();
-
-    {
-        int u = w * 16 + lr;
-        short8_t bM0 = *(const short8_t*)(wdt + u * 128 + lq * 8);
-        short8_t bM1 = *(const short8_t*)(wdt + u * 128 + 32 + lq * 8);
-        short8_t bP0 = *(const short8_t*)(wdt + u * 128 + 64 + lq * 8);
-        short8_t bP1 = *(const short8_t*)(wdt + u * 128 + 96 + lq * 8);
-        const float* aggf = (const float*)aggfU;
-        f32x4 q0 = *(const f32x4*)(aggf + (lr & 3) * 68 + lq * 8);
-        f32x4 q1 = *(const f32x4*)(aggf + (lr & 3) * 68 + lq * 8 + 4);
-        f32x4 q2 = *(const f32x4*)(aggf + (lr & 3) * 68 + 32 + lq * 8);
-        f32x4 q3 = *(const f32x4*)(aggf + (lr & 3) * 68 + 32 + lq * 8 + 4);
-        union { uint uu[4]; short8_t s8; } pc0, pc1;
-        pc0.uu[0] = f2bf2(q0[0], q0[1]); pc0.uu[1] = f2bf2(q0[2], q0[3]);
-        pc0.uu[2] = f2bf2(q1[0], q1[1]); pc0.uu[3] = f2bf2(q1[2], q1[3]);
-        pc1.uu[0] = f2bf2(q2[0], q2[1]); pc1.uu[1] = f2bf2(q2[2], q2[3]);
-        pc1.uu[2] = f2bf2(q3[0], q3[1]); pc1.uu[3] = f2bf2(q3[2], q3[3]);
-        f32x4 aP = {0.f, 0.f, 0.f, 0.f};
-        aP = MFMA_BF16(pc0.s8, bP0, aP, 0, 0, 0);
-        aP = MFMA_BF16(pc1.s8, bP1, aP, 0, 0, 0);
-        f32x4 p2;
-        p2[0] = __shfl(aP[0], lr, 64); p2[1] = __shfl(aP[1], lr, 64);
-        p2[2] = __shfl(aP[2], lr, 64); p2[3] = __shfl(aP[3], lr, 64);
-        f32x4 s1p = {0.f, 0.f, 0.f, 0.f}, s2p = {0.f, 0.f, 0.f, 0.f};
-        f32x4 mx = {-1e30f, -1e30f, -1e30f, -1e30f};
-#pragma unroll
-        for (int mt = 0; mt < 9; ++mt) {
-            const ushort* hrow = h2 + (mt * 16 + lr) * 72;
-            short8_t a0 = *(const short8_t*)(hrow + lq * 8);
-            short8_t a1 = *(const short8_t*)(hrow + 32 + lq * 8);
-            f32x4 acc = {0.f, 0.f, 0.f, 0.f};
-            acc = MFMA_BF16(a0, bM0, acc, 0, 0, 0);
-            acc = MFMA_BF16(a1, bM1, acc, 0, 0, 0);
-            f32x4 mk = *(const f32x4*)(lmask + mt * 16 + lq * 4);
-            f32x4 am = (acc + p2) * mk;
-            s1p += am;
-            s2p += am * am;
-            if (mt < 8) {
-#pragma unroll
-                for (int r = 0; r < 4; ++r) mx[r] = fmaxf(mx[r], am[r]);
-            } else if (lq < 3) {
-#pragma unroll
-                for (int r = 0; r < 4; ++r) mx[r] = fmaxf(mx[r], am[r]);
-            }
-        }
-#pragma unroll
-        for (int r = 0; r < 4; ++r) {
-            mx[r] = fmaxf(mx[r], __shfl_xor(mx[r], 16, 64));
-            mx[r] = fmaxf(mx[r], __shfl_xor(mx[r], 32, 64));
-        }
-        float s1 = s1p[0] + s1p[1] + s1p[2] + s1p[3];
-        float s2 = s2p[0] + s2p[1] + s2p[2] + s2p[3];
-        s1 += __shfl_xor(s1, 16, 64); s1 += __shfl_xor(s1, 32, 64);
-        s2 += __shfl_xor(s2, 16, 64); s2 += __shfl_xor(s2, 32, 64);
-        if (lq == 0) {
-            float sg = (gd[u] < 0.f) ? -1.f : 1.f;
-            float bdu = bd[u];
-#pragma unroll
-            for (int r = 0; r < 4; ++r)
-                m3[(size_t)(k0 + r) * 128 + u] = f2bf(fmaf(sg, mx[r], bdu));
-            int slot = blockIdx.x & 63;
-            atomicAdd(&slot3[slot * 256 + u], s1);
-            atomicAdd(&slot3[slot * 256 + 128 + u], s2);
-        }
-    }
 }
 
 __device__ __forceinline__ void phaseA_leg(
@@ -511,9 +622,9 @@
         int r0 = tid >> 4;
         float g0 = fmaxf(fmaxf(aggp[uu], aggp[32 + uu]),
                          fmaxf(aggp[64 + uu], aggp[96 + uu]));
-        float g1 = fmaxf(fmaxf(aggp[16 + uu], aggp[48 + uu]),
-                         fmaxf(aggp[80 + uu], aggp[112 + uu]));
-        ushort a0 = f2bf(g0), a1b = f2bf(g1);
+        float g1v = fmaxf(fmaxf(aggp[16 + uu], aggp[48 + uu]),
+                          fmaxf(aggp[80 + uu], aggp[112 + uu]));
+        ushort a0 = f2bf(g0), a1b = f2bf(g1v);
 #pragma unroll
         for (int j = 0; j < 5; ++j) {
             int row = r0 + j * 16;
@@ -524,16 +635,48 @@
     __syncthreads();
 }
 
-template <bool WSPATH>
-__global__ __launch_bounds__(256) void k_stage3_full(
+__global__ __launch_bounds__(256) void k_stats2_fb(
+    const float* __restrict__ x,
+    const float* __restrict__ W1, const float* __restrict__ b1,
+    const ushort* __restrict__ w2t,
+    const float* __restrict__ ws,
+    float* __restrict__ slot2) {
+    __shared__ __align__(16) ushort h1[80 * 40];
+    __shared__ float lmask[80];
+    __shared__ float aggp[128];
+    int tid = threadIdx.x;
+    int k0 = blockIdx.x * 2;
+    phaseA_leg(k0, tid, x, W1, b1, ws + PAR_A1, ws + PAR_C1, h1, lmask, aggp);
+    int w = tid >> 6, lane = tid & 63, lq = lane >> 4, lr = lane & 15;
+    int u = w * 16 + lr;
+    short8_t bfrag = *(const short8_t*)(w2t + u * 32 + lq * 8);
+    float s1v = 0.f, s2v = 0.f;
+    float b2skip = 0.f; (void)b2skip;
+#pragma unroll
+    for (int mt = 0; mt < 5; ++mt) {
+        short8_t afrag = *(const short8_t*)(h1 + (mt * 16 + lr) * 40 + lq * 8);
+        f32x4 acc = {0.f, 0.f, 0.f, 0.f};
+        acc = MFMA_BF16(afrag, bfrag, acc, 0, 0, 0);
+#pragma unroll
+        for (int r = 0; r < 4; ++r) { s1v += acc[r]; s2v = fmaf(acc[r], acc[r], s2v); }
+    }
+    s1v += __shfl_xor(s1v, 16, 64); s1v += __shfl_xor(s1v, 32, 64);
+    s2v += __shfl_xor(s2v, 16, 64); s2v += __shfl_xor(s2v, 32, 64);
+    if (lq == 0) {
+        int slot = blockIdx.x & 63;
+        atomicAdd(&slot2[slot * 128 + u], s1v);
+        atomicAdd(&slot2[slot * 128 + 64 + u], s2v);
+    }
+}
+
+__global__ __launch_bounds__(256) void k_stage3_fb(
     const float* __restrict__ x,
     const float* __restrict__ W1, const float* __restrict__ b1,
     const float* __restrict__ b2,
     const ushort* __restrict__ w2t, const ushort* __restrict__ wdt,
     const float* __restrict__ bd, const float* __restrict__ gd,
     const float* __restrict__ ws,
-    float* __restrict__ slot3,
-    ushort* __restrict__ m3, float* __restrict__ outbuf) {
+    float* __restrict__ slot3, float* __restrict__ outbuf) {
     __shared__ __align__(16) ushort h1[80 * 40];
     __shared__ __align__(16) ushort h2[80 * 136];
     __shared__ float lmask[80];
@@ -543,7 +686,6 @@
     int k0 = blockIdx.x * 2;
     int w = tid >> 6, lane = tid & 63, lq = lane >> 4, lr = lane & 15;
     phaseA_leg(k0, tid, x, W1, b1, ws + PAR_A1, ws + PAR_C1, h1, lmask, aggp);
-
     int u0 = w * 32;
     short8_t bfr[2][4];
 #pragma unroll
@@ -551,7 +693,6 @@
 #pragma unroll
         for (int kk = 0; kk < 4; ++kk)
             bfr[s][kk] = *(const short8_t*)(wdt + ((u0 + s * 16 + lr) * 128 + kk * 32 + lq * 8));
-
     {
         int u = w * 16 + lr;
         short8_t bfrag = *(const short8_t*)(w2t + u * 32 + lq * 8);
@@ -576,10 +717,7 @@
         aggv0 = fmaxf(aggv0, __shfl_xor(aggv0, 32, 64));
         aggv1 = fmaxf(aggv1, __shfl_xor(aggv1, 16, 64));
         aggv1 = fmaxf(aggv1, __shfl_xor(aggv1, 32, 64));
-        if (lq == 0) {
-            agg2bf[u] = f2bf(aggv0);
-            agg2bf[64 + u] = f2bf(aggv1);
-        }
+        if (lq == 0) { agg2bf[u] = f2bf(aggv0); agg2bf[64 + u] = f2bf(aggv1); }
     }
     __syncthreads();
     {
@@ -644,45 +782,12 @@
                 float bdu = bd[u];
                 float sg = (gd[u] < 0.f) ? -1.f : 1.f;
 #pragma unroll
-                for (int v = 0; v < 2; ++v) {
-                    float res = fmaf(sg, mxa[s][v], bdu);
-                    if (WSPATH) m3[(size_t)(k0 + v) * 128 + u] = f2bf(res);
-                    else        outbuf[(size_t)u * KVOX + (k0 + v)] = res;
-                }
+                for (int v = 0; v < 2; ++v)
+                    outbuf[(size_t)u * KVOX + (k0 + v)] = fmaf(sg, mxa[s][v], bdu);
                 atomicAdd(&slot3[slot * 256 + u], s1a[s]);
                 atomicAdd(&slot3[slot * 256 + 128 + u], s2a[s]);
             }
         }
-    }
-}
-
-__global__ __launch_bounds__(256) void k_final_ws(const ushort* __restrict__ m3,
-                                                  const float* __restrict__ ws,
-                                                  float* __restrict__ out) {
-    __shared__ float tile[32][33];
-    int tx = threadIdx.x & 31;
-    int ty = threadIdx.x >> 5;
-    int v0 = blockIdx.x * 32;
-    int u0 = blockIdx.y * 32;
-    const float* a3 = ws + PAR_A3;
-    const float* c3 = ws + PAR_C3;
-#pragma unroll
-    for (int r = ty; r < 32; r += 8) {
-        int v = v0 + r, u = u0 + tx;
-        float y = 0.f;
-        if (v < KVOX) {
-            float a = a3[u], c = c3[u];
-            float val = bf2f(m3[(size_t)v * 128 + u]);
-            y = a * val + c;
-            y = (y >= 0.f) ? y : 0.1f * y;
-        }
-        tile[r][tx] = y;
-    }
-    __syncthreads();
-#pragma unroll
-    for (int r = ty; r < 32; r += 8) {
-        int u = u0 + r, v = v0 + tx;
-        if (v < KVOX) out[(size_t)u * KVOX + v] = tile[tx][r];
     }
 }
 
@@ -719,37 +824,35 @@
     ushort* w2t = (ushort*)(ws + W2T_OFF);
     ushort* wdt = (ushort*)(ws + WDT_OFF);
     ushort* m3  = (ushort*)(ws + M3_OFF);
-    uint* recs  = (uint*)(ws + H1G_OFF);
+    uint* recs  = (uint*)(ws + RECS_OFF);
+    uint* bar   = (uint*)(ws + BAR_OFF);
 
     size_t wsf = ws_size / 4;
     bool full = wsf >= (size_t)FULL_FLOATS;
-    bool small = wsf >= (size_t)SMALL_FLOATS;
     const float invN = 1.f / (float)NPTS;
 
     hipMemsetAsync(d_ws, 0, (size_t)STATS_FLOATS * 4, stream);
-
-    k_prep_stats1<<<64 + 256, 256, 0, stream>>>(x, W2, Wd, gd, w2t, wdt, ws + SLOTG_OFF);
-    k_affine1g<<<1, 64, 0, stream>>>(ws + SLOTG_OFF, W1, b1, g1, be1, ws + PAR_A1, ws + PAR_C1, invN);
-    if (full)
-        k_stats2<true><<<KVOX / 4, 512, 0, stream>>>(x, W1, b1, w2t, ws, ws + SLOT2_OFF, recs);
-    else
-        k_stats2<false><<<KVOX / 4, 512, 0, stream>>>(x, W1, b1, w2t, ws, ws + SLOT2_OFF, recs);
-    k_affine_b<<<1, 64, 0, stream>>>(ws + SLOT2_OFF, g2, be2, b2, ws + PAR_A2, ws + PAR_C2, 64, invN);
+    k_prep<<<64, 256, 0, stream>>>(W2, Wd, gd, w2t, wdt);
 
     if (full) {
-        k_stage3_reuse<<<KVOX / 4, 512, 0, stream>>>(recs, b2, w2t, wdt, bd, gd, ws,
-                                                     ws + SLOT3_OFF, m3);
-        k_affine_b3<<<1, 128, 0, stream>>>(ws + SLOT3_OFF, gd, bed, bd, ws + PAR_A3, ws + PAR_C3, 128, invN);
-        k_final_ws<<<dim3((KVOX + 31) / 32, 4), 256, 0, stream>>>(m3, ws, out);
-    } else if (small) {
-        k_stage3_full<true><<<KVOX / 2, 256, 0, stream>>>(x, W1, b1, b2, w2t, wdt, bd, gd, ws,
-                                                          ws + SLOT3_OFF, m3, out);
-        k_affine_b3<<<1, 128, 0, stream>>>(ws + SLOT3_OFF, gd, bed, bd, ws + PAR_A3, ws + PAR_C3, 128, invN);
+        k_fused<<<NBLK, 512, 0, stream>>>(x, W1, b1, g1, be1, b2, g2, be2,
+                                          w2t, wdt, bd, gd,
+                                          ws + SLOTG_OFF, ws + SLOT2_OFF, ws + SLOT3_OFF,
+                                          bar, recs, m3);
+        k_affine_b3<<<1, 128, 0, stream>>>(ws + SLOT3_OFF, gd, bed, bd,
+                                           ws + PAR_A3, ws + PAR_C3, 128, invN);
         k_final_ws<<<dim3((KVOX + 31) / 32, 4), 256, 0, stream>>>(m3, ws, out);
     } else {
-        k_stage3_full<false><<<KVOX / 2, 256, 0, stream>>>(x, W1, b1, b2, w2t, wdt, bd, gd, ws,
-                                                           ws + SLOT3_OFF, m3, out);
-        k_affine_b3<<<1, 128, 0, stream>>>(ws + SLOT3_OFF, gd, bed, bd, ws + PAR_A3, ws + PAR_C3, 128, invN);
+        k_gram<<<256, 256, 0, stream>>>(x, ws + SLOTG_OFF);
+        k_affine1g<<<1, 64, 0, stream>>>(ws + SLOTG_OFF, W1, b1, g1, be1,
+                                         ws + PAR_A1, ws + PAR_C1, invN);
+        k_stats2_fb<<<KVOX / 2, 256, 0, stream>>>(x, W1, b1, w2t, ws, ws + SLOT2_OFF);
+        k_affine_b<<<1, 64, 0, stream>>>(ws + SLOT2_OFF, g2, be2, b2,
+                                         ws + PAR_A2, ws + PAR_C2, 64, invN);
+        k_stage3_fb<<<KVOX / 2, 256, 0, stream>>>(x, W1, b1, b2, w2t, wdt, bd, gd, ws,
+                                                  ws + SLOT3_OFF, out);
+        k_affine_b3<<<1, 128, 0, stream>>>(ws + SLOT3_OFF, gd, bed, bd,
+                                           ws + PAR_A3, ws + PAR_C3, 128, invN);
         k_final_inplace<<<dim3((KVOX + 255) / 256, 128), 256, 0, stream>>>(ws, out);
     }
     hipMemcpyAsync((char*)d_out + (size_t)128 * KVOX * 4, coord,
```

Result: slower. 510.4 us (+231.4%).
